# Optimization experiments

Hardware: AMD Instinct MI355X
Metric: run time of the kernel (lower is better)

Reference implementation:

```python
import jax, jax.numpy as jnp
import numpy as np

BN_EPS = 1e-5


def setup_inputs() -> dict:
    key = jax.random.key(0)
    ks = jax.random.split(key, 16)
    N, E = 50000, 800000
    IN, OUT, EA, EE = 128, 128, 32, 16
    s = lambda k, fi, fo: jax.random.normal(k, (fi, fo), jnp.float32) / np.sqrt(fi)
    return {
        "x": jax.random.normal(ks[0], (N, IN), jnp.float32),
        "edge_attr": jax.random.normal(ks[1], (E, EA), jnp.float32),
        "W_emb": s(ks[2], EA, EE), "b_emb": jnp.zeros((EE,), jnp.float32),
        "W_temb": s(ks[3], EE, OUT), "b_temb": jnp.zeros((OUT,), jnp.float32),
        "W_tattr": s(ks[4], EA, OUT), "b_tattr": jnp.zeros((OUT,), jnp.float32),
        "W_gate": s(ks[5], 3 * OUT, OUT), "b_gate": jnp.zeros((OUT,), jnp.float32),
        "W_l": s(ks[6], IN, OUT), "b_l": jnp.zeros((OUT,), jnp.float32),
        "W_r": s(ks[7], IN, OUT),
        "gamma": jnp.ones((OUT,), jnp.float32), "beta": jnp.zeros((OUT,), jnp.float32),
        "edge_index": jax.random.randint(ks[8], (2, E), 0, N, jnp.int64 if jax.config.jax_enable_x64 else jnp.int32),
    }


def reference(x, edge_attr, W_emb, b_emb, W_temb, b_temb, W_tattr, b_tattr,
              W_gate, b_gate, W_l, b_l, W_r, gamma, beta, edge_index):
    N = x.shape[0]
    row, col = edge_index[0], edge_index[1]

    # edge feature transforms
    emb = jax.nn.relu(edge_attr @ W_emb + b_emb)          # [E, EE]
    t_attr = edge_attr @ W_tattr + b_tattr                # [E, OUT]
    t = (emb @ W_temb + b_temb) + t_attr                  # [E, OUT]

    # SAGEConv (PyG default): mean-aggregate source feats x[row] at target col
    agg = jax.ops.segment_sum(x[row], col, num_segments=N)           # [N, IN]
    cnt = jax.ops.segment_sum(jnp.ones_like(col, x.dtype), col, num_segments=N)
    agg = agg / jnp.maximum(cnt, 1.0)[:, None]
    out = agg @ W_l + b_l + x @ W_r                       # [N, OUT]

    # edge gating: gather out at targets, gate, scatter-add back
    comb = jnp.concatenate([out[col], t, t_attr], axis=-1)  # [E, 3*OUT]
    gate = jax.nn.sigmoid(comb @ W_gate + b_gate)           # [E, OUT]
    out = out + jax.ops.segment_sum(gate * t, col, num_segments=N)

    # BatchNorm1d (training-mode batch stats, biased variance)
    mu = jnp.mean(out, axis=0)
    var = jnp.mean((out - mu) ** 2, axis=0)
    out = (out - mu) * jax.lax.rsqrt(var + BN_EPS) * gamma + beta

    # residual = Identity -> out + out, then relu
    return jax.nn.relu(2.0 * out)
```

## Files before the change

### kernel.cpp

```cpp
#include <hip/hip_runtime.h>
#include <math.h>

#define BN_EPS 1e-5f

typedef short s16x8 __attribute__((ext_vector_type(8)));
typedef float f32x4 __attribute__((ext_vector_type(4)));
#define MFMA16(a, b, c) __builtin_amdgcn_mfma_f32_16x16x32_bf16(a, b, c, 0, 0, 0)

static __device__ __forceinline__ short f2b(float f) {
  union { float f; unsigned u; } x;
  x.f = f;
  unsigned r = (x.u + 0x7fffu + ((x.u >> 16) & 1u)) >> 16;
  return (short)r;
}
static __device__ __forceinline__ float b2f(unsigned bits16) {
  union { unsigned u; float f; } x;
  x.u = bits16 << 16;
  return x.f;
}

__global__ __launch_bounds__(256) void k_prep(
    const float* __restrict__ W_emb, const float* __restrict__ W_tattr,
    const float* __restrict__ W_temb, const float* __restrict__ W_gate,
    short* __restrict__ WembT, short* __restrict__ WtaT,
    short* __restrict__ WteT, short* __restrict__ WgT) {
  int t = blockIdx.x * 256 + threadIdx.x;
  if (t < 512) {
    int c = t >> 5, k = t & 31;
    WembT[t] = f2b(W_emb[k * 16 + c]);
  }
  if (t < 4096) {
    int c = t >> 5, k = t & 31;
    WtaT[t] = f2b(W_tattr[k * 128 + c]);
    WteT[t] = (k < 16) ? f2b(W_temb[k * 128 + c]) : (short)0;
  }
  if (t < 49152) {
    int c = t / 384, k = t % 384;
    WgT[t] = f2b(W_gate[k * 128 + c]);
  }
}

__global__ __launch_bounds__(256) void k_count(
    const int* __restrict__ ei, int* __restrict__ cnt, int E) {
  for (int e = blockIdx.x * blockDim.x + threadIdx.x; e < E;
       e += gridDim.x * blockDim.x)
    atomicAdd(&cnt[ei[E + e]], 1);
}

__global__ __launch_bounds__(1024) void k_scan(
    const int* __restrict__ cnt, int* __restrict__ rowptr,
    int* __restrict__ wo, int N) {
  __shared__ int s[1024];
  __shared__ int carry_s;
  int tid = threadIdx.x;
  if (tid == 0) { carry_s = 0; rowptr[0] = 0; }
  __syncthreads();
  for (int base = 0; base < N; base += 1024) {
    int i = base + tid;
    int v = (i < N) ? cnt[i] : 0;
    s[tid] = v;
    __syncthreads();
#pragma unroll
    for (int off = 1; off < 1024; off <<= 1) {
      int t = (tid >= off) ? s[tid - off] : 0;
      __syncthreads();
      s[tid] += t;
      __syncthreads();
    }
    int inc = s[tid] + carry_s;
    if (i < N) { rowptr[i + 1] = inc; wo[i] = inc - v; }
    __syncthreads();
    if (tid == 1023) carry_s = inc;
    __syncthreads();
  }
}

__global__ __launch_bounds__(256) void k_fill(
    const int* __restrict__ ei, int* __restrict__ wo,
    int* __restrict__ src, int* __restrict__ inv, int E) {
  for (int e = blockIdx.x * blockDim.x + threadIdx.x; e < E;
       e += gridDim.x * blockDim.x) {
    int c = ei[E + e];
    int p = atomicAdd(&wo[c], 1);
    src[p] = ei[e];
    inv[e] = p;
  }
}

__global__ __launch_bounds__(256) void k_agg_gather(
    const float* __restrict__ x, const int* __restrict__ rowptr,
    const int* __restrict__ src, float* __restrict__ agg, int N) {
  int node = blockIdx.x * 4 + (threadIdx.x >> 6);
  if (node >= N) return;
  int l = threadIdx.x & 63;
  int s0 = rowptr[node], s1 = rowptr[node + 1];
  float a0 = 0.f, a1 = 0.f;
  int i = s0;
  for (; i + 1 < s1; i += 2) {
    int sa = src[i], sb = src[i + 1];
    float2 va = reinterpret_cast<const float2*>(x + (size_t)sa * 128)[l];
    float2 vb = reinterpret_cast<const float2*>(x + (size_t)sb * 128)[l];
    a0 += va.x + vb.x;
    a1 += va.y + vb.y;
  }
  if (i < s1) {
    float2 va = reinterpret_cast<const float2*>(x + (size_t)src[i] * 128)[l];
    a0 += va.x;
    a1 += va.y;
  }
  float sc = 1.0f / fmaxf((float)(s1 - s0), 1.0f);
  float2 r = make_float2(a0 * sc, a1 * sc);
  reinterpret_cast<float2*>(agg + (size_t)node * 128)[l] = r;
}

__global__ __launch_bounds__(256) void k_aggregate(
    const float* __restrict__ x, const int* __restrict__ ei,
    float* __restrict__ agg, float* __restrict__ cnt, int N, int E) {
  int total = E * 32;
  for (int idx = blockIdx.x * blockDim.x + threadIdx.x; idx < total;
       idx += gridDim.x * blockDim.x) {
    int e = idx >> 5, c = idx & 31;
    int r = ei[e];
    int d = ei[E + e];
    float4 v = reinterpret_cast<const float4*>(x)[(size_t)r * 32 + c];
    float* dst = agg + (size_t)d * 128 + c * 4;
    unsafeAtomicAdd(dst + 0, v.x);
    unsafeAtomicAdd(dst + 1, v.y);
    unsafeAtomicAdd(dst + 2, v.z);
    unsafeAtomicAdd(dst + 3, v.w);
    if (c == 0) unsafeAtomicAdd(cnt + d, 1.0f);
  }
}

__global__ __launch_bounds__(256) void k_node_linear(
    const float* __restrict__ x, float* __restrict__ agg,
    const float* __restrict__ cntf, const float* __restrict__ Wl,
    const float* __restrict__ bl, const float* __restrict__ Wr,
    float* __restrict__ out_lin, int N, int csr) {
  __shared__ float a_s[32][128];
  __shared__ float x_s[32][128];
  int n0 = blockIdx.x * 32;
  int tid = threadIdx.x;
#pragma unroll
  for (int i = 0; i < 16; ++i) {
    int idx = tid + i * 256;
    int nl = idx >> 7, j = idx & 127;
    int n = n0 + nl;
    float av = 0.f, xv = 0.f;
    if (n < N) {
      size_t off = (size_t)n * 128 + j;
      if (csr) {
        av = agg[off];
      } else {
        av = agg[off] / fmaxf(cntf[n], 1.0f);
        agg[off] = 0.0f;
      }
      xv = x[off];
    }
    a_s[nl][j] = av;
    x_s[nl][j] = xv;
  }
  __syncthreads();
  int j = tid & 127, g = tid >> 7;
  float acc[16];
  float bj = bl[j];
#pragma unroll
  for (int i = 0; i < 16; ++i) acc[i] = bj;
  for (int k = 0; k < 128; ++k) {
    float wl = Wl[k * 128 + j];
    float wr = Wr[k * 128 + j];
#pragma unroll
    for (int i = 0; i < 16; ++i)
      acc[i] += a_s[g * 16 + i][k] * wl + x_s[g * 16 + i][k] * wr;
  }
#pragma unroll
  for (int i = 0; i < 16; ++i) {
    int n = n0 + g * 16 + i;
    if (n < N) out_lin[(size_t)n * 128 + j] = acc[i];
  }
}

template <int MODE>
__global__ __launch_bounds__(256, 3) void k_edge_gate_mfma(
    const float* __restrict__ edge_attr, const int* __restrict__ ei,
    const float* __restrict__ out_lin,
    const short* __restrict__ WembT, const float* __restrict__ b_emb,
    const short* __restrict__ WteT, const float* __restrict__ b_temb,
    const short* __restrict__ WtaT, const float* __restrict__ b_tattr,
    const short* __restrict__ WgT, const float* __restrict__ b_gate,
    float* __restrict__ acc_out, short* __restrict__ et,
    const int* __restrict__ inv, int E) {
  __shared__ short emb_s[64][40];
  __shared__ short comb_s[64][264];
  __shared__ int col_s[64];
  __shared__ int inv_s[64];

  const int tid = threadIdx.x;
  const int w = tid >> 6;
  const int l = tid & 63;
  const int m = l & 15;
  const int g = l >> 4;
  const int e0 = blockIdx.x * 64;
  const int erow = w * 16;

  if (l < 16) {
    col_s[erow + l] = ei[E + e0 + erow + l];
    if (MODE == 1) inv_s[erow + l] = inv[e0 + erow + l];
  }
  {
    int rr = erow + (l >> 2);
    int cc = 16 + (l & 3) * 4;
    int2 zz = make_int2(0, 0);
    *reinterpret_cast<int2*>(&emb_s[rr][cc]) = zz;
  }

  const f32x4 zf = {0.f, 0.f, 0.f, 0.f};

  s16x8 Aea;
  {
    const float* eap = edge_attr + (size_t)(e0 + erow + m) * 32 + g * 8;
    float4 u0 = *reinterpret_cast<const float4*>(eap);
    float4 u1 = *reinterpret_cast<const float4*>(eap + 4);
    Aea[0] = f2b(u0.x); Aea[1] = f2b(u0.y); Aea[2] = f2b(u0.z); Aea[3] = f2b(u0.w);
    Aea[4] = f2b(u1.x); Aea[5] = f2b(u1.y); Aea[6] = f2b(u1.z); Aea[7] = f2b(u1.w);
  }

  {
    s16x8 Bemb = *reinterpret_cast<const s16x8*>(WembT + m * 32 + g * 8);
    f32x4 Demb = MFMA16(Aea, Bemb, zf);
    float be = b_emb[m];
#pragma unroll
    for (int r = 0; r < 4; ++r)
      emb_s[erow + g * 4 + r][m] = f2b(fmaxf(Demb[r] + be, 0.f));
  }

  s16x8 Aemb = *reinterpret_cast<const s16x8*>(&emb_s[erow + m][g * 8]);

  f32x4 ta[8], tt[8];
#pragma unroll
  for (int n = 0; n < 8; ++n) {
    s16x8 B = *reinterpret_cast<const s16x8*>(WtaT + (n * 16 + m) * 32 + g * 8);
    ta[n] = MFMA16(Aea, B, zf);
  }
#pragma unroll
  for (int n = 0; n < 8; ++n) {
    s16x8 B = *reinterpret_cast<const s16x8*>(WteT + (n * 16 + m) * 32 + g * 8);
    tt[n] = MFMA16(Aemb, B, ta[n]);
  }
#pragma unroll
  for (int n = 0; n < 8; ++n) {
    float bta = b_tattr[n * 16 + m];
    float bte = b_temb[n * 16 + m];
#pragma unroll
    for (int r = 0; r < 4; ++r) {
      float tav = ta[n][r] + bta;
      float tv = tt[n][r] + bta + bte;
      tt[n][r] = tv;
      comb_s[erow + g * 4 + r][n * 16 + m] = f2b(tv);
      comb_s[erow + g * 4 + r][128 + n * 16 + m] = f2b(tav);
    }
  }

  s16x8 Ag[12];
  {
    int cd = col_s[erow + m];
    const float* op = out_lin + (size_t)cd * 128 + g * 8;
#pragma unroll
    for (int kc = 0; kc < 4; ++kc) {
      float4 v0 = *reinterpret_cast<const float4*>(op + kc * 32);
      float4 v1 = *reinterpret_cast<const float4*>(op + kc * 32 + 4);
      s16x8 a;
      a[0] = f2b(v0.x); a[1] = f2b(v0.y); a[2] = f2b(v0.z); a[3] = f2b(v0.w);
      a[4] = f2b(v1.x); a[5] = f2b(v1.y); a[6] = f2b(v1.z); a[7] = f2b(v1.w);
      Ag[kc] = a;
    }
  }
#pragma unroll
  for (int kc = 0; kc < 8; ++kc)
    Ag[4 + kc] = *reinterpret_cast<const s16x8*>(&comb_s[erow + m][kc * 32 + g * 8]);

  int dD[4];
#pragma unroll
  for (int r = 0; r < 4; ++r)
    dD[r] = (MODE == 1) ? inv_s[erow + g * 4 + r] : col_s[erow + g * 4 + r];

#pragma unroll
  for (int n = 0; n < 8; ++n) {
    f32x4 acc = zf;
    const short* bp = WgT + (n * 16 + m) * 384 + g * 8;
#pragma unroll
    for (int kc = 0; kc < 12; ++kc)
      acc = MFMA16(Ag[kc], *reinterpret_cast<const s16x8*>(bp + kc * 32), acc);
    float bg = b_gate[n * 16 + m];
#pragma unroll
    for (int r = 0; r < 4; ++r) {
      float gate = 1.f / (1.f + __expf(-(acc[r] + bg)));
      float val = gate * tt[n][r];
      if (MODE == 1) {
        et[(size_t)dD[r] * 128 + n * 16 + m] = f2b(val);
      } else {
        unsafeAtomicAdd(acc_out + (size_t)dD[r] * 128 + n * 16 + m, val);
      }
    }
  }
}

__global__ __launch_bounds__(256) void k_gate_gather(
    const short* __restrict__ et, const int* __restrict__ rowptr,
    float* __restrict__ out, int N) {
  int node = blockIdx.x * 4 + (threadIdx.x >> 6);
  if (node >= N) return;
  int l = threadIdx.x & 63;
  int s0 = rowptr[node], s1 = rowptr[node + 1];
  float a0 = 0.f, a1 = 0.f;
  const unsigned* ep = reinterpret_cast<const unsigned*>(et);
  int i = s0;
  for (; i + 1 < s1; i += 2) {
    unsigned ua = ep[(size_t)i * 64 + l];
    unsigned ub = ep[(size_t)(i + 1) * 64 + l];
    a0 += b2f(ua & 0xffffu) + b2f(ub & 0xffffu);
    a1 += b2f(ua >> 16) + b2f(ub >> 16);
  }
  if (i < s1) {
    unsigned ua = ep[(size_t)i * 64 + l];
    a0 += b2f(ua & 0xffffu);
    a1 += b2f(ua >> 16);
  }
  float2* op = reinterpret_cast<float2*>(out + (size_t)node * 128);
  float2 v = op[l];
  v.x += a0;
  v.y += a1;
  op[l] = v;
}

__global__ __launch_bounds__(256) void k_bn_stats(
    const float* __restrict__ out_lin, const float* __restrict__ acc,
    float* __restrict__ bn, int N) {
  int j = threadIdx.x & 127;
  int g = threadIdx.x >> 7;
  float s = 0.f, s2 = 0.f;
  for (int n = blockIdx.x * 2 + g; n < N; n += gridDim.x * 2) {
    size_t off = (size_t)n * 128 + j;
    float v = out_lin[off];
    if (acc) v += acc[off];
    s += v;
    s2 += v * v;
  }
  unsafeAtomicAdd(&bn[j], s);
  unsafeAtomicAdd(&bn[128 + j], s2);
}

__global__ __launch_bounds__(256) void k_finalize(
    float* __restrict__ out, const float* __restrict__ acc,
    const float* __restrict__ bn, const float* __restrict__ gamma,
    const float* __restrict__ beta, int N) {
  int total = N * 32;
  float invN = 1.0f / (float)N;
  for (int idx = blockIdx.x * blockDim.x + threadIdx.x; idx < total;
       idx += gridDim.x * blockDim.x) {
    int q = idx & 31;
    float4 v = reinterpret_cast<float4*>(out)[idx];
    float4 a = acc ? reinterpret_cast<const float4*>(acc)[idx]
                   : make_float4(0.f, 0.f, 0.f, 0.f);
    float* vp = &v.x;
    const float* ap = &a.x;
    float4 r;
    float* rp = &r.x;
#pragma unroll
    for (int c = 0; c < 4; ++c) {
      int j = q * 4 + c;
      float mu = bn[j] * invN;
      float var = bn[128 + j] * invN - mu * mu;
      float val = vp[c] + ap[c];
      float y = (val - mu) * rsqrtf(var + BN_EPS) * gamma[j] + beta[j];
      rp[c] = fmaxf(2.f * y, 0.f);
    }
    reinterpret_cast<float4*>(out)[idx] = r;
  }
}

extern "C" void kernel_launch(void* const* d_in, const int* in_sizes, int n_in,
                              void* d_out, int out_size, void* d_ws, size_t ws_size,
                              hipStream_t stream) {
  const float* x       = (const float*)d_in[0];
  const float* ea      = (const float*)d_in[1];
  const float* W_emb   = (const float*)d_in[2];
  const float* b_emb   = (const float*)d_in[3];
  const float* W_temb  = (const float*)d_in[4];
  const float* b_temb  = (const float*)d_in[5];
  const float* W_tattr = (const float*)d_in[6];
  const float* b_tattr = (const float*)d_in[7];
  const float* W_gate  = (const float*)d_in[8];
  const float* b_gate  = (const float*)d_in[9];
  const float* W_l     = (const float*)d_in[10];
  const float* b_l     = (const float*)d_in[11];
  const float* W_r     = (const float*)d_in[12];
  const float* gamma   = (const float*)d_in[13];
  const float* beta    = (const float*)d_in[14];
  const int*   eidx    = (const int*)d_in[15];

  int N = in_sizes[0] / 128;
  int E = in_sizes[1] / 32;
  float* out = (float*)d_out;
  char* base = (char*)d_ws;

  size_t o = 0;
  auto take = [&](size_t b) { size_t r = o; o = (o + b + 255) & ~(size_t)255; return r; };
  size_t o_agg    = take((size_t)N * 128 * 4);
  size_t o_cnt    = take((size_t)N * 4);
  size_t o_rowptr = take((size_t)(N + 1) * 4);
  size_t o_wo     = take((size_t)N * 4);
  size_t o_src    = take((size_t)E * 4);
  size_t o_inv    = take((size_t)E * 4);
  size_t o_bn     = take(256 * 4);
  size_t o_wb     = take(57856 * 2);
  size_t o_et     = take((size_t)E * 128 * 2);
  bool csr = (ws_size >= o);

  if (csr) {
    float* agg    = (float*)(base + o_agg);
    int*   cnt    = (int*)(base + o_cnt);
    int*   rowptr = (int*)(base + o_rowptr);
    int*   wo     = (int*)(base + o_wo);
    int*   src    = (int*)(base + o_src);
    int*   inv    = (int*)(base + o_inv);
    float* bn     = (float*)(base + o_bn);
    short* wb     = (short*)(base + o_wb);
    short* WembT  = wb;
    short* WtaT   = wb + 512;
    short* WteT   = wb + 4608;
    short* WgT    = wb + 8704;
    short* et     = (short*)(base + o_et);

    hipMemsetAsync(cnt, 0, (size_t)N * 4, stream);
    hipMemsetAsync(bn, 0, 256 * 4, stream);

    k_prep<<<192, 256, 0, stream>>>(W_emb, W_tattr, W_temb, W_gate,
                                    WembT, WtaT, WteT, WgT);
    k_count<<<512, 256, 0, stream>>>(eidx, cnt, E);
    k_scan<<<1, 1024, 0, stream>>>(cnt, rowptr, wo, N);
    k_fill<<<512, 256, 0, stream>>>(eidx, wo, src, inv, E);
    k_agg_gather<<<(N + 3) / 4, 256, 0, stream>>>(x, rowptr, src, agg, N);
    k_node_linear<<<(N + 31) / 32, 256, 0, stream>>>(x, agg, nullptr, W_l, b_l,
                                                     W_r, out, N, 1);
    k_edge_gate_mfma<1><<<E / 64, 256, 0, stream>>>(
        ea, eidx, out, WembT, b_emb, WteT, b_temb, WtaT, b_tattr, WgT, b_gate,
        nullptr, et, inv, E);
    k_gate_gather<<<(N + 3) / 4, 256, 0, stream>>>(et, rowptr, out, N);
    k_bn_stats<<<512, 256, 0, stream>>>(out, nullptr, bn, N);
    k_finalize<<<2048, 256, 0, stream>>>(out, nullptr, bn, gamma, beta, N);
  } else {
    float* agg  = (float*)d_ws;
    float* cntf = agg + (size_t)N * 128;
    float* bn   = cntf + N;
    short* wb   = (short*)(bn + 256);
    short* WembT = wb;
    short* WtaT  = wb + 512;
    short* WteT  = wb + 4608;
    short* WgT   = wb + 8704;

    size_t zero_bytes = ((size_t)N * 128 + N + 256) * sizeof(float);
    hipMemsetAsync(d_ws, 0, zero_bytes, stream);

    k_prep<<<192, 256, 0, stream>>>(W_emb, W_tattr, W_temb, W_gate,
                                    WembT, WtaT, WteT, WgT);
    k_aggregate<<<2048, 256, 0, stream>>>(x, eidx, agg, cntf, N, E);
    k_node_linear<<<(N + 31) / 32, 256, 0, stream>>>(x, agg, cntf, W_l, b_l,
                                                     W_r, out, N, 0);
    k_edge_gate_mfma<0><<<E / 64, 256, 0, stream>>>(
        ea, eidx, out, WembT, b_emb, WteT, b_temb, WtaT, b_tattr, WgT, b_gate,
        agg, nullptr, nullptr, E);
    k_bn_stats<<<512, 256, 0, stream>>>(out, agg, bn, N);
    k_finalize<<<2048, 256, 0, stream>>>(out, agg, bn, gamma, beta, N);
  }
}
```

Measured before the change: 1.292 ms.

## Fold t and t_attr gate weights algebraically to shrink gate GEMM K

Because t = emb@W_temb + t_attr + biases, the gate GEMM over [out, t, t_attr] is rewritten as out@W1 + t_attr@(W2+W3) + emb@(W_temb@W2), plus a folded bias. The edge kernel then runs 9 MFMA steps per output tile instead of 12 and stages only t_attr in LDS, halving comb_s. That smaller LDS and register footprint allows raising the occupancy hint from 3 to 4. The prep kernel now does a small weight-by-weight product, and the bf16 rounding of the combined weights differs slightly from before.

```diff
diff --git a/kernel.cpp b/kernel.cpp
--- a/kernel.cpp
+++ b/kernel.cpp
@@ -20,23 +20,42 @@
 }
 
 __global__ __launch_bounds__(256) void k_prep(
-    const float* __restrict__ W_emb, const float* __restrict__ W_tattr,
-    const float* __restrict__ W_temb, const float* __restrict__ W_gate,
+    const float* __restrict__ We, const float* __restrict__ Wta,
+    const float* __restrict__ Wte, const float* __restrict__ Wg,
+    const float* __restrict__ bta, const float* __restrict__ bte,
+    const float* __restrict__ bg,
     short* __restrict__ WembT, short* __restrict__ WtaT,
-    short* __restrict__ WteT, short* __restrict__ WgT) {
+    short* __restrict__ WteT, short* __restrict__ B1,
+    short* __restrict__ B23, short* __restrict__ Bem,
+    float* __restrict__ bgf) {
   int t = blockIdx.x * 256 + threadIdx.x;
   if (t < 512) {
     int c = t >> 5, k = t & 31;
-    WembT[t] = f2b(W_emb[k * 16 + c]);
+    WembT[t] = f2b(We[k * 16 + c]);
   }
   if (t < 4096) {
     int c = t >> 5, k = t & 31;
-    WtaT[t] = f2b(W_tattr[k * 128 + c]);
-    WteT[t] = (k < 16) ? f2b(W_temb[k * 128 + c]) : (short)0;
-  }
-  if (t < 49152) {
-    int c = t / 384, k = t % 384;
-    WgT[t] = f2b(W_gate[k * 128 + c]);
+    WtaT[t] = f2b(Wta[k * 128 + c]);
+    WteT[t] = (k < 16) ? f2b(Wte[k * 128 + c]) : (short)0;
+  }
+  if (t < 16384) {
+    int c = t >> 7, k = t & 127;
+    B1[t] = f2b(Wg[k * 128 + c]);
+    B23[t] = f2b(Wg[(128 + k) * 128 + c] + Wg[(256 + k) * 128 + c]);
+  }
+  if (t < 4096) {
+    int c = t >> 5, k = t & 31;
+    float s = 0.f;
+    if (k < 16)
+      for (int j = 0; j < 128; ++j) s += Wte[k * 128 + j] * Wg[(128 + j) * 128 + c];
+    Bem[t] = (k < 16) ? f2b(s) : (short)0;
+  }
+  if (t < 128) {
+    float s = bg[t];
+    for (int j = 0; j < 128; ++j)
+      s += (bta[j] + bte[j]) * Wg[(128 + j) * 128 + t] +
+           bta[j] * Wg[(256 + j) * 128 + t];
+    bgf[t] = s;
   }
 }
 
@@ -181,17 +200,18 @@
 }
 
 template <int MODE>
-__global__ __launch_bounds__(256, 3) void k_edge_gate_mfma(
+__global__ __launch_bounds__(256, 4) void k_edge_gate_mfma(
     const float* __restrict__ edge_attr, const int* __restrict__ ei,
     const float* __restrict__ out_lin,
     const short* __restrict__ WembT, const float* __restrict__ b_emb,
     const short* __restrict__ WteT, const float* __restrict__ b_temb,
     const short* __restrict__ WtaT, const float* __restrict__ b_tattr,
-    const short* __restrict__ WgT, const float* __restrict__ b_gate,
+    const short* __restrict__ B1, const short* __restrict__ B23,
+    const short* __restrict__ Bem, const float* __restrict__ bgf,
     float* __restrict__ acc_out, short* __restrict__ et,
     const int* __restrict__ inv, int E) {
   __shared__ short emb_s[64][40];
-  __shared__ short comb_s[64][264];
+  __shared__ short comb_s[64][132];
   __shared__ int col_s[64];
   __shared__ int inv_s[64];
 
@@ -249,19 +269,16 @@
   }
 #pragma unroll
   for (int n = 0; n < 8; ++n) {
-    float bta = b_tattr[n * 16 + m];
-    float bte = b_temb[n * 16 + m];
+    float bta_ = b_tattr[n * 16 + m];
+    float bte_ = b_temb[n * 16 + m];
 #pragma unroll
     for (int r = 0; r < 4; ++r) {
-      float tav = ta[n][r] + bta;
-      float tv = tt[n][r] + bta + bte;
-      tt[n][r] = tv;
-      comb_s[erow + g * 4 + r][n * 16 + m] = f2b(tv);
-      comb_s[erow + g * 4 + r][128 + n * 16 + m] = f2b(tav);
+      comb_s[erow + g * 4 + r][n * 16 + m] = f2b(ta[n][r]);
+      tt[n][r] = tt[n][r] + bta_ + bte_;
     }
   }
 
-  s16x8 Ag[12];
+  s16x8 Ago[4];
   {
     int cd = col_s[erow + m];
     const float* op = out_lin + (size_t)cd * 128 + g * 8;
@@ -272,12 +289,13 @@
       s16x8 a;
       a[0] = f2b(v0.x); a[1] = f2b(v0.y); a[2] = f2b(v0.z); a[3] = f2b(v0.w);
       a[4] = f2b(v1.x); a[5] = f2b(v1.y); a[6] = f2b(v1.z); a[7] = f2b(v1.w);
-      Ag[kc] = a;
+      Ago[kc] = a;
     }
   }
-#pragma unroll
-  for (int kc = 0; kc < 8; ++kc)
-    Ag[4 + kc] = *reinterpret_cast<const s16x8*>(&comb_s[erow + m][kc * 32 + g * 8]);
+  s16x8 Agt[4];
+#pragma unroll
+  for (int kc = 0; kc < 4; ++kc)
+    Agt[kc] = *reinterpret_cast<const s16x8*>(&comb_s[erow + m][kc * 32 + g * 8]);
 
   int dD[4];
 #pragma unroll
@@ -286,15 +304,20 @@
 
 #pragma unroll
   for (int n = 0; n < 8; ++n) {
+    const short* b1p = B1 + (n * 16 + m) * 128 + g * 8;
+    const short* b23p = B23 + (n * 16 + m) * 128 + g * 8;
     f32x4 acc = zf;
-    const short* bp = WgT + (n * 16 + m) * 384 + g * 8;
-#pragma unroll
-    for (int kc = 0; kc < 12; ++kc)
-      acc = MFMA16(Ag[kc], *reinterpret_cast<const s16x8*>(bp + kc * 32), acc);
-    float bg = b_gate[n * 16 + m];
+#pragma unroll
+    for (int kc = 0; kc < 4; ++kc)
+      acc = MFMA16(Ago[kc], *reinterpret_cast<const s16x8*>(b1p + kc * 32), acc);
+#pragma unroll
+    for (int kc = 0; kc < 4; ++kc)
+      acc = MFMA16(Agt[kc], *reinterpret_cast<const s16x8*>(b23p + kc * 32), acc);
+    acc = MFMA16(Aemb, *reinterpret_cast<const s16x8*>(Bem + (n * 16 + m) * 32 + g * 8), acc);
+    float bg_ = bgf[n * 16 + m];
 #pragma unroll
     for (int r = 0; r < 4; ++r) {
-      float gate = 1.f / (1.f + __expf(-(acc[r] + bg)));
+      float gate = 1.f / (1.f + __expf(-(acc[r] + bg_)));
       float val = gate * tt[n][r];
       if (MODE == 1) {
         et[(size_t)dD[r] * 128 + n * 16 + m] = f2b(val);
@@ -404,6 +427,8 @@
   float* out = (float*)d_out;
   char* base = (char*)d_ws;
 
+  const size_t WB_SHORTS = 512 + 4096 + 4096 + 16384 + 16384 + 4096;
+
   size_t o = 0;
   auto take = [&](size_t b) { size_t r = o; o = (o + b + 255) & ~(size_t)255; return r; };
   size_t o_agg    = take((size_t)N * 128 * 4);
@@ -413,7 +438,8 @@
   size_t o_src    = take((size_t)E * 4);
   size_t o_inv    = take((size_t)E * 4);
   size_t o_bn     = take(256 * 4);
-  size_t o_wb     = take(57856 * 2);
+  size_t o_wb     = take(WB_SHORTS * 2);
+  size_t o_bgf    = take(128 * 4);
   size_t o_et     = take((size_t)E * 128 * 2);
   bool csr = (ws_size >= o);
 
@@ -429,14 +455,18 @@
     short* WembT  = wb;
     short* WtaT   = wb + 512;
     short* WteT   = wb + 4608;
-    short* WgT    = wb + 8704;
+    short* B1     = wb + 8704;
+    short* B23    = wb + 25088;
+    short* Bem    = wb + 41472;
+    float* bgf    = (float*)(base + o_bgf);
     short* et     = (short*)(base + o_et);
 
     hipMemsetAsync(cnt, 0, (size_t)N * 4, stream);
     hipMemsetAsync(bn, 0, 256 * 4, stream);
 
-    k_prep<<<192, 256, 0, stream>>>(W_emb, W_tattr, W_temb, W_gate,
-                                    WembT, WtaT, WteT, WgT);
+    k_prep<<<64, 256, 0, stream>>>(W_emb, W_tattr, W_temb, W_gate,
+                                   b_tattr, b_temb, b_gate,
+                                   WembT, WtaT, WteT, B1, B23, Bem, bgf);
     k_count<<<512, 256, 0, stream>>>(eidx, cnt, E);
     k_scan<<<1, 1024, 0, stream>>>(cnt, rowptr, wo, N);
     k_fill<<<512, 256, 0, stream>>>(eidx, wo, src, inv, E);
@@ -444,8 +474,8 @@
     k_node_linear<<<(N + 31) / 32, 256, 0, stream>>>(x, agg, nullptr, W_l, b_l,
                                                      W_r, out, N, 1);
     k_edge_gate_mfma<1><<<E / 64, 256, 0, stream>>>(
-        ea, eidx, out, WembT, b_emb, WteT, b_temb, WtaT, b_tattr, WgT, b_gate,
-        nullptr, et, inv, E);
+        ea, eidx, out, WembT, b_emb, WteT, b_temb, WtaT, b_tattr,
+        B1, B23, Bem, bgf, nullptr, et, inv, E);
     k_gate_gather<<<(N + 3) / 4, 256, 0, stream>>>(et, rowptr, out, N);
     k_bn_stats<<<512, 256, 0, stream>>>(out, nullptr, bn, N);
     k_finalize<<<2048, 256, 0, stream>>>(out, nullptr, bn, gamma, beta, N);
@@ -457,19 +487,23 @@
     short* WembT = wb;
     short* WtaT  = wb + 512;
     short* WteT  = wb + 4608;
-    short* WgT   = wb + 8704;
+    short* B1    = wb + 8704;
+    short* B23   = wb + 25088;
+    short* Bem   = wb + 41472;
+    float* bgf   = (float*)(wb + WB_SHORTS + (WB_SHORTS & 1));
 
     size_t zero_bytes = ((size_t)N * 128 + N + 256) * sizeof(float);
     hipMemsetAsync(d_ws, 0, zero_bytes, stream);
 
-    k_prep<<<192, 256, 0, stream>>>(W_emb, W_tattr, W_temb, W_gate,
-                                    WembT, WtaT, WteT, WgT);
+    k_prep<<<64, 256, 0, stream>>>(W_emb, W_tattr, W_temb, W_gate,
+                                   b_tattr, b_temb, b_gate,
+                                   WembT, WtaT, WteT, B1, B23, Bem, bgf);
     k_aggregate<<<2048, 256, 0, stream>>>(x, eidx, agg, cntf, N, E);
     k_node_linear<<<(N + 31) / 32, 256, 0, stream>>>(x, agg, cntf, W_l, b_l,
                                                      W_r, out, N, 0);
     k_edge_gate_mfma<0><<<E / 64, 256, 0, stream>>>(
-        ea, eidx, out, WembT, b_emb, WteT, b_temb, WtaT, b_tattr, WgT, b_gate,
-        agg, nullptr, nullptr, E);
+        ea, eidx, out, WembT, b_emb, WteT, b_temb, WtaT, b_tattr,
+        B1, B23, Bem, bgf, agg, nullptr, nullptr, E);
     k_bn_stats<<<512, 256, 0, stream>>>(out, agg, bn, N);
     k_finalize<<<2048, 256, 0, stream>>>(out, agg, bn, gamma, beta, N);
   }
```

After: 1.209 ms. 1.07x faster.
